# Performance work log

Measured on AMD Instinct MI355X. Metric: run time of the kernel, lower is better.

Reference implementation:

```python
import jax, jax.numpy as jnp
import numpy as np

NUM_TOKENS = 8192
TOKEN_DIM = 256
N = 65536
TOPK = 5
DECAY = 0.1      # cur_decay (set_decay_updates never called -> stays at init decay)
EPS = 1e-5
TEMP = 1.0


def setup_inputs() -> dict:
    key = jax.random.key(0)
    k1, k2 = jax.random.split(key)
    return {
        "inputs_flatten": jax.random.normal(k1, (N, TOKEN_DIM), dtype=jnp.float32),
        "embed": jax.random.normal(k2, (NUM_TOKENS, TOKEN_DIM), dtype=jnp.float32),
        "cluster_size": jnp.zeros((NUM_TOKENS,), dtype=jnp.float32),
        "cluster_sum": jnp.zeros((NUM_TOKENS,), dtype=jnp.float32),
        "embed_avg": jnp.zeros((NUM_TOKENS, TOKEN_DIM), dtype=jnp.float32),
    }


def reference(inputs_flatten, embed, cluster_size, cluster_sum, embed_avg):
    x = inputs_flatten                              # [N, D]
    # squared euclidean distances to codebook: [N, K]
    distances = (jnp.sum(x * x, axis=1, keepdims=True)
                 + jnp.sum(embed * embed, axis=1)
                 - 2.0 * (x @ embed.T))
    # top-k nearest codes (smallest distance)
    neg_topk, topk_idx = jax.lax.top_k(-distances, TOPK)   # [N, k]
    topk_dist = -neg_topk
    weights = jax.nn.softmax(-topk_dist / TEMP, axis=1)    # [N, k]
    # scatter soft weights into dense one-hot-ish encodings [N, K]
    rows = jnp.arange(x.shape[0])[:, None]
    encodings = jnp.zeros_like(distances).at[rows, topk_idx].set(weights)
    encoding_indices = jnp.argmax(encodings, axis=1)[:, None]   # [N, 1]

    # training-mode EMA codebook update (module default is training=True)
    encoding_sum = jnp.sum(encodings, axis=0)                   # [K]
    new_cluster_sum = cluster_sum + encoding_sum
    new_cluster_size = cluster_size * DECAY + encoding_sum * (1.0 - DECAY)
    embed_sum = encodings.T @ x                                 # [K, D]
    new_embed_avg = embed_avg * DECAY + embed_sum * (1.0 - DECAY)
    smoothed = (new_cluster_size + EPS) / (jnp.sum(new_cluster_size) + NUM_TOKENS * EPS)
    cs = smoothed * jnp.sum(new_cluster_size)
    new_embed = new_embed_avg / cs[:, None]                     # embed.data.copy_(...)

    quantize = encodings @ new_embed                            # [N, D]
    quantize = jax.lax.stop_gradient(quantize - x) + x          # straight-through
    return quantize, encoding_indices
```

## Files before the change

kernel.cpp:

```cpp
#include <hip/hip_runtime.h>
#include <hip/hip_bf16.h>
#include <math.h>
#include <limits.h>

#define NROWS 65536
#define DIM   256
#define NCODE 8192
#define NTOPK 5

typedef __attribute__((ext_vector_type(4))) float     f32x4;
typedef __attribute__((ext_vector_type(4))) int       i32x4;

#define WS_ESWZ   0u
#define WS_CINIT  2097152u
#define WS_XQ     2129920u
#define WS_NEWEMB 2129920u
#define WS_ENTR   10518528u
#define WS_IDX5   18907136u
#define WS_W5     20217856u
#define WS_ENCSUM 21528576u
#define WS_CNT    21561344u
#define WS_OFFS   21594112u
#define WS_CURS   21626880u
#define WS_SFAC   21659648u

#define ENT_PER_BLK 64
#define NENT (NROWS * NTOPK)

__device__ __forceinline__ void gl_lds16(const void* g, void* l) {
  __builtin_amdgcn_global_load_lds(
      (const __attribute__((address_space(1))) unsigned int*)g,
      (__attribute__((address_space(3))) unsigned int*)l, 16, 0, 0);
}

__device__ __forceinline__ unsigned f2key(float f) {
  unsigned u = __float_as_uint(f);
  return (u & 0x80000000u) ? ~u : (u | 0x80000000u);
}
__device__ __forceinline__ float key2f(unsigned k) {
  unsigned u = (k & 0x80000000u) ? (k ^ 0x80000000u) : ~k;
  return __uint_as_float(u);
}

__device__ __forceinline__ int pk4(f32x4 v) {
  int r = 0;
  #pragma unroll
  for (int j = 0; j < 4; ++j) {
    float q = fminf(127.f, fmaxf(-127.f, rintf(16.f * v[j])));
    r |= ((int)q & 255) << (8 * j);
  }
  return r;
}

__global__ __launch_bounds__(256) void k_prep(const float* __restrict__ embed,
                                              signed char* __restrict__ eswz,
                                              int* __restrict__ cinit) {
  const int code = blockIdx.x;
  const int d = threadIdx.x;
  float v = embed[code * DIM + d];
  float qf = fminf(127.f, fmaxf(-127.f, rintf(16.f * v)));
  int q = (int)qf;
  __shared__ unsigned char rb[256];
  __shared__ int red[4];
  rb[d] = (unsigned char)(q & 255);
  int e2 = q * q;
  #pragma unroll
  for (int off = 32; off; off >>= 1) e2 += __shfl_down(e2, off);
  const int lane = d & 63, w = d >> 6;
  if (lane == 0) red[w] = e2;
  __syncthreads();
  if (d == 0) {
    int s = red[0] + red[1] + red[2] + red[3];
    cinit[code] = -(s >> 1) * 8192 + code;
  }
  if (d < 64) {
    unsigned u = (unsigned)rb[4 * d] | ((unsigned)rb[4 * d + 1] << 8) |
                 ((unsigned)rb[4 * d + 2] << 16) | ((unsigned)rb[4 * d + 3] << 24);
    const int cs = (d >> 2) ^ (code & 15);
    ((unsigned*)(eswz + code * 256))[(cs << 2) | (d & 3)] = u;
  }
}

__global__ __launch_bounds__(256) void k_prepx(const float* __restrict__ x,
                                               signed char* __restrict__ xq) {
  const int t = threadIdx.x;
  const int s = t >> 6, q = (t >> 4) & 3, ln = t & 15;
  const unsigned row0 = blockIdx.x * 64;
  #pragma unroll
  for (int g = 0; g < 4; ++g) {
    const unsigned row = row0 + g * 16 + ln;
    const float* xr = x + row * DIM + s * 64 + q * 16;
    i32x4 dw;
    #pragma unroll
    for (int d = 0; d < 4; ++d) dw[d] = pk4(*(const f32x4*)(xr + d * 4));
    *(i32x4*)(xq + (unsigned)(row0 + g * 16) * 256u + (unsigned)t * 16u) = dw;
  }
}


struct PList { int a, b, c, d; };

__device__ __forceinline__ void ladder(PList& P, int t) {
  int c0 = min(P.a, t); P.a = max(P.a, t);
  int c1 = min(P.b, c0); P.b = max(P.b, c0);
  int c2 = min(P.c, c1); P.c = max(P.c, c1);
  P.d = max(P.d, c2);
}

__device__ __forceinline__ void psel(PList& P, i32x4 acc, i32x4 en) {
  int p0 = acc[0] * 8192 + en[0];
  int p1 = acc[1] * 8192 + en[1];
  int p2 = acc[2] * 8192 + en[2];
  int p3 = acc[3] * 8192 + en[3];
  int h1 = max(p0, p1);
  int h2 = max(p2, p3);
  int t1 = max(h1, h2);
  if (__any(t1 > P.d)) {
    int l1 = min(p0, p1), l2 = min(p2, p3);
    int t2 = max(min(h1, h2), max(l1, l2));
    ladder(P, t1);
    if (__any(t2 > P.d)) ladder(P, t2);
  }
}

#define GBODY(IT, SL, NS)                                                      \
  {                                                                            \
    const int tl = ((IT) + 2 < 64) ? (IT) + 2 : 63;                            \
    const signed char* src = esw_h + (unsigned)tl * 8192u;                     \
    gl_lds16(src + tid * 16, &ebuf[NS][tid * 16]);                             \
    gl_lds16(src + 4096 + tid * 16, &ebuf[NS][4096 + tid * 16]);               \
    i32x4 enC0 = *(const i32x4*)(cin_h + tl * 32 + q * 4);                     \
    i32x4 enC1 = *(const i32x4*)(cin_h + tl * 32 + 16 + q * 4);                \
    asm volatile("s_waitcnt vmcnt(8)\n\ts_barrier" ::: "memory");              \
    const signed char* eb = ebuf[SL];                                          \
    i32x4 a00 = {0, 0, 0, 0}, a01 = a00, a10 = a00, a11 = a00;                 \
    __builtin_amdgcn_s_setprio(1);                                             \
    _Pragma("unroll")                                                          \
    for (int s = 0; s < 4; ++s) {                                              \
      const int chunk = (4 * s + q) ^ ln;                                      \
      i32x4 ea0 = *(const i32x4*)&eb[ln * 256 + chunk * 16];                   \
      i32x4 ea1 = *(const i32x4*)&eb[4096 + ln * 256 + chunk * 16];            \
      a00 = __builtin_amdgcn_mfma_i32_16x16x64_i8(ea0, xf[0][s], a00, 0, 0, 0);\
      a10 = __builtin_amdgcn_mfma_i32_16x16x64_i8(ea0, xf[1][s], a10, 0, 0, 0);\
      a01 = __builtin_amdgcn_mfma_i32_16x16x64_i8(ea1, xf[0][s], a01, 0, 0, 0);\
      a11 = __builtin_amdgcn_mfma_i32_16x16x64_i8(ea1, xf[1][s], a11, 0, 0, 0);\
    }                                                                          \
    __builtin_amdgcn_s_setprio(0);                                             \
    psel(P0, a00, enA0); psel(P0, a01, enA1);                                  \
    psel(P1, a10, enA0); psel(P1, a11, enA1);                                  \
    enA0 = enB0; enA1 = enB1; enB0 = enC0; enB1 = enC1;                        \
  }

__global__ __launch_bounds__(256, 4) void k_gemm(const signed char* __restrict__ xq,
                                                 const signed char* __restrict__ eswz,
                                                 const int* __restrict__ cinit,
                                                 int* __restrict__ candk) {
  __shared__ signed char ebuf[4][8192];
  const int tid = threadIdx.x;
  const int lane = tid & 63, wave = tid >> 6;
  const int q = lane >> 4, ln = lane & 15;
  const int quarter = blockIdx.x & 3, rblk = blockIdx.x >> 2;
  const int wrow0 = rblk * 128 + wave * 32;
  const signed char* esw_h = eswz + (unsigned)quarter * (2048u * 256u);
  const int* cin_h = cinit + quarter * 2048;

  gl_lds16(esw_h + tid * 16, &ebuf[0][tid * 16]);
  gl_lds16(esw_h + 4096 + tid * 16, &ebuf[0][4096 + tid * 16]);
  gl_lds16(esw_h + 8192 + tid * 16, &ebuf[1][tid * 16]);
  gl_lds16(esw_h + 8192 + 4096 + tid * 16, &ebuf[1][4096 + tid * 16]);
  i32x4 enA0 = *(const i32x4*)(cin_h + q * 4);
  i32x4 enA1 = *(const i32x4*)(cin_h + 16 + q * 4);
  i32x4 enB0 = *(const i32x4*)(cin_h + 32 + q * 4);
  i32x4 enB1 = *(const i32x4*)(cin_h + 48 + q * 4);

  i32x4 xf[2][4];
  {
    const signed char* xb = xq + (unsigned)wrow0 * 256u;
    #pragma unroll
    for (int t = 0; t < 2; ++t)
      #pragma unroll
      for (int s = 0; s < 4; ++s)
        xf[t][s] = *(const i32x4*)(xb + t * 4096 + s * 1024 + lane * 16);
  }

  PList P0 = {INT_MIN, INT_MIN, INT_MIN, INT_MIN};
  PList P1 = P0;

  #pragma unroll 1
  for (int ob = 0; ob < 16; ++ob) {
    const int it0 = ob * 4;
    GBODY(it0 + 0, 0, 2)
    GBODY(it0 + 1, 1, 3)
    GBODY(it0 + 2, 2, 0)
    GBODY(it0 + 3, 3, 1)
  }

  {
    const int row0 = wrow0 + ln;
    i32x4 pk0 = {P0.a, P0.b, P0.c, P0.d};
    *(i32x4*)&candk[row0 * 64 + quarter * 16 + q * 4] = pk0;
    const int row1 = wrow0 + 16 + ln;
    i32x4 pk1 = {P1.a, P1.b, P1.c, P1.d};
    *(i32x4*)&candk[row1 * 64 + quarter * 16 + q * 4] = pk1;
  }
}

__global__ __launch_bounds__(256) void k_refine(const float* __restrict__ x,
                                                const float* __restrict__ embed,
                                                const int* __restrict__ candk,
                                                float* __restrict__ out_idx,
                                                int* __restrict__ idx5,
                                                float* __restrict__ w5,
                                                float* __restrict__ enc_sum,
                                                unsigned* __restrict__ cnt) {
  __shared__ float sh[4][8][66];
  const int wave = threadIdx.x >> 6, l = threadIdx.x & 63;
  const int row = blockIdx.x * 4 + wave;

  int k = candk[row * 64 + l];
  int cd[8];
  #pragma unroll
  for (int j = 0; j < 8; ++j) {
    int m = k;
    #pragma unroll
    for (int off = 1; off < 64; off <<= 1) m = max(m, __shfl_xor(m, off));
    cd[j] = m & 8191;
    if (k == m) k = INT_MIN;
  }

  const float* xr = x + (unsigned)row * DIM;
  const f32x4 xv = *(const f32x4*)(xr + 4 * l);
  const float t0 = -2.f * xv[0], t1 = -2.f * xv[1];
  const float t2 = -2.f * xv[2], t3 = -2.f * xv[3];

  #pragma unroll
  for (int ci = 0; ci < 8; ++ci) {
    const f32x4 e = *(const f32x4*)(embed + (unsigned)cd[ci] * DIM + 4 * l);
    float p = e[0] * (e[0] + t0);
    p = fmaf(e[1], e[1] + t1, p);
    p = fmaf(e[2], e[2] + t2, p);
    p = fmaf(e[3], e[3] + t3, p);
    sh[wave][ci][l] = p;
  }
  asm volatile("s_waitcnt lgkmcnt(0)" ::: "memory");

  const int c = l >> 3, sub = l & 7;
  const float* sp = &sh[wave][c][sub * 8];
  f32x4 v0 = *(const f32x4*)sp;
  f32x4 v1 = *(const f32x4*)(sp + 4);
  double s64 = (double)v0[0] + (double)v0[1] + (double)v0[2] + (double)v0[3]
             + (double)v1[0] + (double)v1[1] + (double)v1[2] + (double)v1[3];
  s64 += __shfl_xor(s64, 1);
  s64 += __shfl_xor(s64, 2);
  s64 += __shfl_xor(s64, 4);

  double sc = __shfl(s64, (l & 7) * 8);
  unsigned fkey = f2key((float)sc);
  const int myc = cd[l & 7];

  bool used = false;
  int codes[5]; float svals[5];
  #pragma unroll
  for (int j = 0; j < 5; ++j) {
    unsigned kk = used ? 0xFFFFFFFFu : fkey;
    unsigned mm = kk;
    #pragma unroll
    for (int off = 1; off < 8; off <<= 1) mm = min(mm, (unsigned)__shfl_xor((int)mm, off));
    int cc = (kk == mm) ? myc : 0x7FFFFFFF;
    #pragma unroll
    for (int off = 1; off < 8; off <<= 1) cc = min(cc, __shfl_xor(cc, off));
    used = used || (myc == cc);
    codes[j] = cc;
    svals[j] = key2f(mm);
  }

  float ex[5], sum = 0.f;
  #pragma unroll
  for (int j = 0; j < 5; ++j) { ex[j] = expf(-(svals[j] - svals[0])); sum += ex[j]; }
  const float inv = 1.f / sum;

  if (l == 0) {
    out_idx[row] = (float)codes[0];
    #pragma unroll
    for (int j = 0; j < 5; ++j) {
      float w = ex[j] * inv;
      idx5[row * 5 + j] = codes[j];
      w5[row * 5 + j] = w;
      atomicAdd(&enc_sum[codes[j]], w);
      atomicAdd(&cnt[codes[j]], 1u);
    }
  }
}

__global__ __launch_bounds__(256) void k_scan(const unsigned* __restrict__ cnt,
                                              unsigned* __restrict__ offs,
                                              unsigned* __restrict__ cursor,
                                              const float* __restrict__ enc_sum,
                                              const float* __restrict__ cluster_size,
                                              float* __restrict__ sfac) {
  __shared__ unsigned part[256];
  __shared__ double sred[256];
  const int t = threadIdx.x;
  unsigned s = 0;
  for (int i = 0; i < 32; ++i) s += cnt[t * 32 + i];
  part[t] = s;
  double ds = 0.0;
  for (int i = t; i < NCODE; i += 256)
    ds += 0.1 * (double)cluster_size[i] + 0.9 * (double)enc_sum[i];
  sred[t] = ds;
  __syncthreads();
  if (t == 0) {
    unsigned run = 0;
    for (int i = 0; i < 256; ++i) { unsigned tmp = part[i]; part[i] = run; run += tmp; }
    double S = 0.0;
    for (int i = 0; i < 256; ++i) S += sred[i];
    sfac[0] = (float)(S / (S + (double)NCODE * 1e-5));
  }
  __syncthreads();
  unsigned off = part[t];
  for (int i = 0; i < 32; ++i) {
    unsigned c = cnt[t * 32 + i];
    offs[t * 32 + i] = off;
    cursor[t * 32 + i] = off;
    off += c;
  }
}

__global__ __launch_bounds__(256) void k_fill(const int* __restrict__ idx5,
                                              const float* __restrict__ w5,
                                              unsigned* __restrict__ cursor,
                                              uint2* __restrict__ entries) {
  const int i = blockIdx.x * 256 + threadIdx.x;
  if (i >= NENT) return;
  const unsigned c = (unsigned)idx5[i];
  const float w = w5[i];
  const unsigned row = (unsigned)i / 5u;
  const unsigned slot = atomicAdd(&cursor[c], 1u);
  entries[slot] = make_uint2((c << 16) | row, __float_as_uint(w));
}

__global__ __launch_bounds__(256) void k_accum2(const float* __restrict__ x,
                                                const uint2* __restrict__ entries,
                                                float* __restrict__ embsum) {
  __shared__ uint2 ent[ENT_PER_BLK];
  const int t = threadIdx.x;
  const unsigned base = blockIdx.x * ENT_PER_BLK;
  if (t < ENT_PER_BLK * 2)
    ((unsigned*)ent)[t] = ((const unsigned*)(entries + base))[t];
  __syncthreads();

  float acc = 0.f;
  unsigned cur = ent[0].x >> 16;
  #pragma unroll 8
  for (int i = 0; i < ENT_PER_BLK; ++i) {
    const uint2 e = ent[i];
    const unsigned code = e.x >> 16;
    const unsigned row = e.x & 0xFFFFu;
    const float w = __uint_as_float(e.y);
    if (code != cur) {
      atomicAdd(&embsum[cur * DIM + t], acc);
      acc = 0.f; cur = code;
    }
    acc = fmaf(w, x[row * DIM + t], acc);
  }
  atomicAdd(&embsum[cur * DIM + t], acc);
}

__global__ __launch_bounds__(256) void k_norm(const float* __restrict__ embed_avg,
                                              const float* __restrict__ cluster_size,
                                              const float* __restrict__ enc_sum,
                                              const float* __restrict__ sfac,
                                              float* __restrict__ embsum ) {
  const int k = blockIdx.x, d = threadIdx.x;
  const float ncs = 0.1f * cluster_size[k] + 0.9f * enc_sum[k];
  const float cs = (ncs + 1e-5f) * sfac[0];
  const unsigned o = (unsigned)k * DIM + d;
  embsum[o] = (0.1f * embed_avg[o] + 0.9f * embsum[o]) / cs;
}

__global__ __launch_bounds__(256) void k_quant(const int* __restrict__ idx5,
                                               const float* __restrict__ w5,
                                               const float* __restrict__ newemb,
                                               float* __restrict__ out) {
  const int d = threadIdx.x;
  const int rb = blockIdx.x * 16;
  #pragma unroll 2
  for (int r = 0; r < 16; ++r) {
    const int row = rb + r;
    float acc = 0.f;
    #pragma unroll
    for (int j = 0; j < 5; ++j)
      acc = fmaf(w5[row * 5 + j], newemb[(unsigned)idx5[row * 5 + j] * DIM + d], acc);
    out[(unsigned)row * DIM + d] = acc;
  }
}

extern "C" void kernel_launch(void* const* d_in, const int* in_sizes, int n_in,
                              void* d_out, int out_size, void* d_ws, size_t ws_size,
                              hipStream_t stream) {
  const float* x            = (const float*)d_in[0];
  const float* embed        = (const float*)d_in[1];
  const float* cluster_size = (const float*)d_in[2];
  const float* embed_avg    = (const float*)d_in[4];

  char* w = (char*)d_ws;
  signed char*    eswz   = (signed char*)(w + WS_ESWZ);
  int*            cinit  = (int*)(w + WS_CINIT);
  signed char*    xq     = (signed char*)(w + WS_XQ);
  int*            idx5   = (int*)(w + WS_IDX5);
  float*          w5     = (float*)(w + WS_W5);
  float*          encsum = (float*)(w + WS_ENCSUM);
  unsigned*       cnt    = (unsigned*)(w + WS_CNT);
  unsigned*       offs   = (unsigned*)(w + WS_OFFS);
  unsigned*       curs   = (unsigned*)(w + WS_CURS);
  float*          sfac   = (float*)(w + WS_SFAC);
  float*          embsum = (float*)(w + WS_NEWEMB);
  uint2*          entr   = (uint2*)(w + WS_ENTR);

  float* out_q   = (float*)d_out;
  float* out_idx = out_q + (size_t)NROWS * DIM;
  int*   candk   = (int*)d_out;

  hipMemsetAsync(w + WS_ENCSUM, 0, 65536, stream);

  k_prep<<<NCODE, 256, 0, stream>>>(embed, eswz, cinit);
  k_prepx<<<NROWS / 64, 256, 0, stream>>>(x, xq);
  k_gemm<<<NROWS / 128 * 4, 256, 0, stream>>>(xq, eswz, cinit, candk);
  hipMemsetAsync(w + WS_NEWEMB, 0, (size_t)NCODE * DIM * 4, stream);
  k_refine<<<NROWS / 4, 256, 0, stream>>>(x, embed, candk, out_idx, idx5, w5, encsum, cnt);
  k_scan<<<1, 256, 0, stream>>>(cnt, offs, curs, encsum, cluster_size, sfac);
  k_fill<<<(NENT + 255) / 256, 256, 0, stream>>>(idx5, w5, curs, entr);
  k_accum2<<<NENT / ENT_PER_BLK, 256, 0, stream>>>(x, entr, embsum);
  k_norm<<<NCODE, 256, 0, stream>>>(embed_avg, cluster_size, encsum, sfac, embsum);
  k_quant<<<NROWS / 16, 256, 0, stream>>>(idx5, w5, embsum, out_q);
}
```

Measured before the change: 435.6 us.

## Trim gemm register pressure, parallelize scan reductions, vectorize quant kernel

The int8 GEMM kernel now prefetches code norms only one tile ahead, using two ping-pong register sets instead of three. It seeds the first MFMA with a zero operand and waits on fewer outstanding loads. Launch bounds rise to 5 waves per SIMD to raise occupancy. The scan kernel swaps its serial single-thread prefix sum and reduction for log-step parallel versions, and the quantize kernel uses float4 loads and stores with four rows per wave. Together these reduce register pressure, serial work and memory instruction count, at the risk of exposing load latency in the GEMM.

```diff
diff --git a/kernel.cpp b/kernel.cpp
--- a/kernel.cpp
+++ b/kernel.cpp
@@ -123,20 +123,30 @@
   }
 }
 
-#define GBODY(IT, SL, NS)                                                      \
+#define GBODY(IT, SL, NS, ENC, ENN)                                            \
   {                                                                            \
-    const int tl = ((IT) + 2 < 64) ? (IT) + 2 : 63;                            \
-    const signed char* src = esw_h + (unsigned)tl * 8192u;                     \
+    const int tg = ((IT) + 2 < 64) ? (IT) + 2 : 63;                            \
+    const int te = ((IT) + 1 < 64) ? (IT) + 1 : 63;                            \
+    const signed char* src = esw_h + (unsigned)tg * 8192u;                     \
     gl_lds16(src + tid * 16, &ebuf[NS][tid * 16]);                             \
     gl_lds16(src + 4096 + tid * 16, &ebuf[NS][4096 + tid * 16]);               \
-    i32x4 enC0 = *(const i32x4*)(cin_h + tl * 32 + q * 4);                     \
-    i32x4 enC1 = *(const i32x4*)(cin_h + tl * 32 + 16 + q * 4);                \
-    asm volatile("s_waitcnt vmcnt(8)\n\ts_barrier" ::: "memory");              \
+    ENN##0 = *(const i32x4*)(cin_h + te * 32 + q * 4);                         \
+    ENN##1 = *(const i32x4*)(cin_h + te * 32 + 16 + q * 4);                    \
+    asm volatile("s_waitcnt vmcnt(4)\n\ts_barrier" ::: "memory");              \
     const signed char* eb = ebuf[SL];                                          \
-    i32x4 a00 = {0, 0, 0, 0}, a01 = a00, a10 = a00, a11 = a00;                 \
+    i32x4 a00, a01, a10, a11;                                                  \
     __builtin_amdgcn_s_setprio(1);                                             \
+    {                                                                          \
+      const int chunk = q ^ ln;                                                \
+      i32x4 ea0 = *(const i32x4*)&eb[ln * 256 + chunk * 16];                   \
+      i32x4 ea1 = *(const i32x4*)&eb[4096 + ln * 256 + chunk * 16];            \
+      a00 = __builtin_amdgcn_mfma_i32_16x16x64_i8(ea0, xf[0][0], ZV, 0, 0, 0); \
+      a10 = __builtin_amdgcn_mfma_i32_16x16x64_i8(ea0, xf[1][0], ZV, 0, 0, 0); \
+      a01 = __builtin_amdgcn_mfma_i32_16x16x64_i8(ea1, xf[0][0], ZV, 0, 0, 0); \
+      a11 = __builtin_amdgcn_mfma_i32_16x16x64_i8(ea1, xf[1][0], ZV, 0, 0, 0); \
+    }                                                                          \
     _Pragma("unroll")                                                          \
-    for (int s = 0; s < 4; ++s) {                                              \
+    for (int s = 1; s < 4; ++s) {                                              \
       const int chunk = (4 * s + q) ^ ln;                                      \
       i32x4 ea0 = *(const i32x4*)&eb[ln * 256 + chunk * 16];                   \
       i32x4 ea1 = *(const i32x4*)&eb[4096 + ln * 256 + chunk * 16];            \
@@ -146,12 +156,11 @@
       a11 = __builtin_amdgcn_mfma_i32_16x16x64_i8(ea1, xf[1][s], a11, 0, 0, 0);\
     }                                                                          \
     __builtin_amdgcn_s_setprio(0);                                             \
-    psel(P0, a00, enA0); psel(P0, a01, enA1);                                  \
-    psel(P1, a10, enA0); psel(P1, a11, enA1);                                  \
-    enA0 = enB0; enA1 = enB1; enB0 = enC0; enB1 = enC1;                        \
-  }
-
-__global__ __launch_bounds__(256, 4) void k_gemm(const signed char* __restrict__ xq,
+    psel(P0, a00, ENC##0); psel(P0, a01, ENC##1);                              \
+    psel(P1, a10, ENC##0); psel(P1, a11, ENC##1);                              \
+  }
+
+__global__ __launch_bounds__(256, 5) void k_gemm(const signed char* __restrict__ xq,
                                                  const signed char* __restrict__ eswz,
                                                  const int* __restrict__ cinit,
                                                  int* __restrict__ candk) {
@@ -170,8 +179,8 @@
   gl_lds16(esw_h + 8192 + 4096 + tid * 16, &ebuf[1][4096 + tid * 16]);
   i32x4 enA0 = *(const i32x4*)(cin_h + q * 4);
   i32x4 enA1 = *(const i32x4*)(cin_h + 16 + q * 4);
-  i32x4 enB0 = *(const i32x4*)(cin_h + 32 + q * 4);
-  i32x4 enB1 = *(const i32x4*)(cin_h + 48 + q * 4);
+  i32x4 enB0 = {0, 0, 0, 0}, enB1 = {0, 0, 0, 0};
+  const i32x4 ZV = {0, 0, 0, 0};
 
   i32x4 xf[2][4];
   {
@@ -189,10 +198,10 @@
   #pragma unroll 1
   for (int ob = 0; ob < 16; ++ob) {
     const int it0 = ob * 4;
-    GBODY(it0 + 0, 0, 2)
-    GBODY(it0 + 1, 1, 3)
-    GBODY(it0 + 2, 2, 0)
-    GBODY(it0 + 3, 3, 1)
+    GBODY(it0 + 0, 0, 2, enA, enB)
+    GBODY(it0 + 1, 1, 3, enB, enA)
+    GBODY(it0 + 2, 2, 0, enA, enB)
+    GBODY(it0 + 3, 3, 1, enB, enA)
   }
 
   {
@@ -309,20 +318,28 @@
     ds += 0.1 * (double)cluster_size[i] + 0.9 * (double)enc_sum[i];
   sred[t] = ds;
   __syncthreads();
+  #pragma unroll
+  for (int off = 1; off < 256; off <<= 1) {
+    unsigned v = (t >= off) ? part[t - off] : 0u;
+    __syncthreads();
+    part[t] += v;
+    __syncthreads();
+  }
+  #pragma unroll
+  for (int off = 128; off; off >>= 1) {
+    if (t < off) sred[t] += sred[t + off];
+    __syncthreads();
+  }
   if (t == 0) {
-    unsigned run = 0;
-    for (int i = 0; i < 256; ++i) { unsigned tmp = part[i]; part[i] = run; run += tmp; }
-    double S = 0.0;
-    for (int i = 0; i < 256; ++i) S += sred[i];
+    double S = sred[0];
     sfac[0] = (float)(S / (S + (double)NCODE * 1e-5));
   }
-  __syncthreads();
-  unsigned off = part[t];
+  unsigned off0 = part[t] - s;
   for (int i = 0; i < 32; ++i) {
     unsigned c = cnt[t * 32 + i];
-    offs[t * 32 + i] = off;
-    cursor[t * 32 + i] = off;
-    off += c;
+    offs[t * 32 + i] = off0;
+    cursor[t * 32 + i] = off0;
+    off0 += c;
   }
 }
 
@@ -382,16 +399,23 @@
                                                const float* __restrict__ w5,
                                                const float* __restrict__ newemb,
                                                float* __restrict__ out) {
-  const int d = threadIdx.x;
+  const int l = threadIdx.x & 63, wv = threadIdx.x >> 6;
   const int rb = blockIdx.x * 16;
-  #pragma unroll 2
-  for (int r = 0; r < 16; ++r) {
-    const int row = rb + r;
-    float acc = 0.f;
-    #pragma unroll
-    for (int j = 0; j < 5; ++j)
-      acc = fmaf(w5[row * 5 + j], newemb[(unsigned)idx5[row * 5 + j] * DIM + d], acc);
-    out[(unsigned)row * DIM + d] = acc;
+  #pragma unroll
+  for (int r = 0; r < 4; ++r) {
+    const int row = rb + wv * 4 + r;
+    f32x4 acc = {0.f, 0.f, 0.f, 0.f};
+    #pragma unroll
+    for (int j = 0; j < 5; ++j) {
+      const int c = idx5[row * 5 + j];
+      const float wg = w5[row * 5 + j];
+      const f32x4 e = *(const f32x4*)(newemb + (unsigned)c * DIM + 4 * l);
+      acc[0] = fmaf(wg, e[0], acc[0]);
+      acc[1] = fmaf(wg, e[1], acc[1]);
+      acc[2] = fmaf(wg, e[2], acc[2]);
+      acc[3] = fmaf(wg, e[3], acc[3]);
+    }
+    *(f32x4*)(out + (unsigned)row * DIM + 4 * l) = acc;
   }
 }
 
```

New measurement: 426.1 us. -2.2%, faster.
